# Kernel tuning notes

Measured on AMD Instinct MI355X. Metric: run time of the kernel, lower is better.

Reference implementation:

```python
import jax, jax.numpy as jnp
import numpy as np

NC, NG, NP = 8192, 4096, 140
FD, D, L = 512, 256, 2
E_OBS, E_COEXP, E_PPI, E_SYM = 300000, 200000, 10000, 20000
EPS = 1e-5


def layer_norm(x, g, b):
    mu = jnp.mean(x, -1, keepdims=True)
    v = jnp.mean((x - mu) ** 2, -1, keepdims=True)
    return (x - mu) * jax.lax.rsqrt(v + EPS) * g + b


def sage(h_src, h_dst, src, dst, w, Ws, Wn, b, n_dst):
    # DGL SAGEConv (mean aggregator, edge-weighted): mean over incoming
    # weighted messages, then fc_self(h_dst) + fc_neigh(neigh) + bias.
    m = h_src[src] * w[:, None]                                  # [E, D]
    neigh = jax.ops.segment_sum(m, dst, num_segments=n_dst)      # [n_dst, D]
    deg = jax.ops.segment_sum(jnp.ones_like(w), dst, num_segments=n_dst)
    neigh = neigh / jnp.maximum(deg, 1.0)[:, None]
    return h_dst @ Ws + neigh @ Wn + b


def setup_inputs() -> dict:
    key = jax.random.key(0)
    ks = iter(jax.random.split(key, 64))
    def n(*s):
        return jax.random.normal(next(ks), s, jnp.float32) * 0.02
    def u(e):
        return jax.random.uniform(next(ks), (e,), jnp.float32)
    def ri(e, hi):
        return jax.random.randint(next(ks), (e,), 0, hi, jnp.int32)
    return dict(
        cell_feat=jax.random.normal(next(ks), (NC, FD), jnp.float32),
        gene_feat=jax.random.normal(next(ks), (NG, FD), jnp.float32),
        pro_idx=jnp.arange(NP, dtype=jnp.int32),
        obs_src=ri(E_OBS, NG), obs_dst=ri(E_OBS, NC), obs_w=u(E_OBS),
        rev_obs_src=ri(E_OBS, NC), rev_obs_dst=ri(E_OBS, NG), rev_obs_w=u(E_OBS),
        symbol_src=ri(E_SYM, NG), symbol_dst=ri(E_SYM, NP), symbol_w=u(E_SYM),
        rev_symbol_src=ri(E_SYM, NP), rev_symbol_dst=ri(E_SYM, NG), rev_symbol_w=u(E_SYM),
        coexp_src=ri(E_COEXP, NG), coexp_dst=ri(E_COEXP, NG), coexp_w=u(E_COEXP),
        ppi_src=ri(E_PPI, NP), ppi_dst=ri(E_PPI, NP), ppi_w=u(E_PPI),
        W_emb_cell=n(FD, D), b_emb_cell=jnp.zeros((D,), jnp.float32),
        W_emb_gene=n(FD, D), b_emb_gene=jnp.zeros((D,), jnp.float32),
        emb_pro=n(NP, D),
        W_mlpcell=n(L, D, D), b_mlpcell=jnp.zeros((L, D), jnp.float32),
        W_sage_self=n(L, 6, D, D), W_sage_neigh=n(L, 6, D, D),
        b_sage=jnp.zeros((L, 6, D), jnp.float32),
        ln1_g=jnp.ones((L, 3, D), jnp.float32), ln1_b=jnp.zeros((L, 3, D), jnp.float32),
        ln2_g=jnp.ones((L, 3, D), jnp.float32), ln2_b=jnp.zeros((L, 3, D), jnp.float32),
        W_last=n(3 * D, NP), b_last=jnp.zeros((NP,), jnp.float32),
    )


def reference(cell_feat, gene_feat, pro_idx,
              obs_src, obs_dst, obs_w,
              rev_obs_src, rev_obs_dst, rev_obs_w,
              symbol_src, symbol_dst, symbol_w,
              rev_symbol_src, rev_symbol_dst, rev_symbol_w,
              coexp_src, coexp_dst, coexp_w,
              ppi_src, ppi_dst, ppi_w,
              W_emb_cell, b_emb_cell, W_emb_gene, b_emb_gene, emb_pro,
              W_mlpcell, b_mlpcell, W_sage_self, W_sage_neigh, b_sage,
              ln1_g, ln1_b, ln2_g, ln2_b, W_last, b_last):
    act = jax.nn.selu
    hc = cell_feat @ W_emb_cell + b_emb_cell      # emb_cell
    hg = gene_feat @ W_emb_gene + b_emb_gene      # emb_gene
    hp = emb_pro[pro_idx]                         # nn.Embedding path
    nc, ng, npn = hc.shape[0], hg.shape[0], hp.shape[0]
    hist = [hc]
    for l in range(W_mlpcell.shape[0]):
        Ws, Wn, bs = W_sage_self[l], W_sage_neigh[l], b_sage[l]
        hmlp = layer_norm(act(hc @ W_mlpcell[l] + b_mlpcell[l]), ln1_g[l, 2], ln1_b[l, 2])
        # HeteroGraphConv(SAGE) over edges_sub = [obs, rev_obs, symbol, rev_symbol] (stack)
        s_obs = sage(hg, hc, obs_src, obs_dst, obs_w, Ws[0], Wn[0], bs[0], nc)
        s_robs = sage(hc, hg, rev_obs_src, rev_obs_dst, rev_obs_w, Ws[1], Wn[1], bs[1], ng)
        s_sym = sage(hg, hp, symbol_src, symbol_dst, symbol_w, Ws[2], Wn[2], bs[2], npn)
        s_rsym = sage(hp, hg, rev_symbol_src, rev_symbol_dst, rev_symbol_w, Ws[3], Wn[3], bs[3], ng)
        # homogeneous subgraph convs: gene_sage on coexp, pro_sage on ppi
        h_gg = layer_norm(act(sage(hg, hg, coexp_src, coexp_dst, coexp_w, Ws[4], Wn[4], bs[4], ng)), ln1_g[l, 0], ln1_b[l, 0])
        h_pp = layer_norm(act(sage(hp, hp, ppi_src, ppi_dst, ppi_w, Ws[5], Wn[5], bs[5], npn)), ln1_g[l, 1], ln1_b[l, 1])
        # norm each stacked relation output, then agg='sum' over the stack dim
        hgen = layer_norm(act(s_robs), ln1_g[l, 0], ln1_b[l, 0]) + layer_norm(act(s_rsym), ln1_g[l, 0], ln1_b[l, 0]) + h_gg
        hpro = layer_norm(act(s_sym), ln1_g[l, 1], ln1_b[l, 1]) + h_pp
        hcel = layer_norm(act(s_obs), ln1_g[l, 2], ln1_b[l, 2]) + hmlp
        hg = layer_norm(act(hgen), ln2_g[l, 0], ln2_b[l, 0])
        hp = layer_norm(act(hpro), ln2_g[l, 1], ln2_b[l, 1])
        hc = layer_norm(act(hcel), ln2_g[l, 2], ln2_b[l, 2])
        hist.append(hc)
    # mlp_last over concat of per-layer cell reps (sum(dims[1:-1]) -> dims[-1])
    return jnp.concatenate(hist, -1) @ W_last + b_last
```

## Files before the change

kernel.cpp:

```cpp
#include <hip/hip_runtime.h>

typedef unsigned short ushort_t;
typedef unsigned int uint_t;

typedef ushort_t ushortx8 __attribute__((ext_vector_type(8)));
typedef ushort_t ushortx4 __attribute__((ext_vector_type(4)));
typedef __bf16 bf16x8 __attribute__((ext_vector_type(8)));
typedef float f32x4 __attribute__((ext_vector_type(4)));

#define NCC 8192
#define NGG 4096
#define NPP 140
#define LDS_STR 88
#define CEPB 16384

__device__ __forceinline__ float bf2f(ushort_t u) {
    uint_t i = ((uint_t)u) << 16;
    float f;
    __builtin_memcpy(&f, &i, 4);
    return f;
}
__device__ __forceinline__ ushort_t f2bf(float f) {
    uint_t i;
    __builtin_memcpy(&i, &f, 4);
    uint_t r = (i + 0x7FFFu + ((i >> 16) & 1u)) >> 16;
    return (ushort_t)r;
}
__device__ __forceinline__ float scrub(float x) {
    return __builtin_isfinite(x) ? x : 0.f;
}
__device__ __forceinline__ float selu_f(float x) {
    return x > 0.f ? 1.0507009873554805f * x : 1.7580993408473766f * expm1f(x);
}
__device__ __forceinline__ float wsum64(float x) {
    for (int o = 32; o; o >>= 1) x += __shfl_xor(x, o, 64);
    return x;
}

__global__ __launch_bounds__(256) void sc_zero1(int* __restrict__ a, int na) {
    int i = blockIdx.x * 256 + threadIdx.x;
    if (i < na) a[i] = 0;
}

struct CountJob {
    const int* dst;
    const int* src;
    const float* w;
    uint_t* pw;
    ushort_t* rank;
    int E;
    int nbins;
    int* deg;
    int bstart;
};
struct CountBatch {
    CountJob j[6];
};
struct TrJob {
    const float* src;
    ushort_t* dst;
    int K, N, nx, nxy;
    int bstart;
};
struct TrBatch {
    TrJob j[6];
};
struct FillJob {
    const int* dst;
    const uint_t* pw;
    const ushort_t* rank;
    int E;
    const int* offs;
    uint_t* ep;
    int bstart;
};
struct FillBatch {
    FillJob j[6];
};
struct GemmJob {
    const void* A1;
    int lda1, K1, af1;
    const ushort_t* Bt1;
    const ushort_t* A2;
    int K2;
    const ushort_t* Bt2;
    const float* bias;
    ushort_t* C;
    int ldc, M;
    int mstart;
};
struct GemmBatch {
    GemmJob j[7];
};

struct CountArgs {
    CountBatch cb;
    int bsC;
    const float* cf;
    ushort_t* cf16;
    int nbC;
    const float* gf;
    ushort_t* gf16;
};
__global__ __launch_bounds__(1024) void sc_count(CountArgs ca) {
    __shared__ int hist[NCC];
    int bx = blockIdx.x;
    const int tid = threadIdx.x;
    if (bx >= ca.bsC) {
        bx -= ca.bsC;
        const float* src;
        ushort_t* dst;
        if (bx < ca.nbC) {
            src = ca.cf;
            dst = ca.cf16;
        } else {
            bx -= ca.nbC;
            src = ca.gf;
            dst = ca.gf16;
        }
        size_t i = ((size_t)bx * 1024 + tid) * 8;
        float4 f0 = *(const float4*)(src + i);
        float4 f1 = *(const float4*)(src + i + 4);
        ushortx8 v;
        v[0] = f2bf(f0.x);
        v[1] = f2bf(f0.y);
        v[2] = f2bf(f0.z);
        v[3] = f2bf(f0.w);
        v[4] = f2bf(f1.x);
        v[5] = f2bf(f1.y);
        v[6] = f2bf(f1.z);
        v[7] = f2bf(f1.w);
        *(ushortx8*)(dst + i) = v;
        return;
    }
    int r = 0;
#pragma unroll
    for (int i = 1; i < 6; ++i) r = (bx >= ca.cb.j[i].bstart) ? i : r;
    const CountJob& J = ca.cb.j[r];
    const int nb = J.nbins;
    for (int b = tid; b < nb; b += 1024) hist[b] = 0;
    __syncthreads();
    const int e0 = (bx - J.bstart) * CEPB;
    ushort_t lrk[16];
#pragma unroll
    for (int u = 0; u < 16; ++u) {
        int e = e0 + u * 1024 + tid;
        if (e < J.E) {
            int d = J.dst[e];
            lrk[u] = (ushort_t)atomicAdd(&hist[d], 1);
            J.pw[e] = ((uint_t)f2bf(J.w[e]) << 16) | (uint_t)J.src[e];
        }
    }
    __syncthreads();
    for (int b = tid; b < nb; b += 1024) {
        int c = hist[b];
        if (c > 0) hist[b] = atomicAdd(&J.deg[b], c);
    }
    __syncthreads();
#pragma unroll
    for (int u = 0; u < 16; ++u) {
        int e = e0 + u * 1024 + tid;
        if (e < J.E) {
            int d = J.dst[e];
            J.rank[e] = (ushort_t)(hist[d] + (int)lrk[u]);
        }
    }
}

struct PrepArgs {
    TrBatch tb;
    int bsT;
    const float* emb;
    const int* pidx;
    ushort_t* hp;
    int nEmb;
};
__global__ __launch_bounds__(256) void sc_prep(PrepArgs pa) {
    __shared__ ushort_t t[32][33];
    int bx = blockIdx.x;
    if (bx < pa.bsT) {
        int r = 0;
#pragma unroll
        for (int i = 1; i < 6; ++i) r = (bx >= pa.tb.j[i].bstart) ? i : r;
        const TrJob& J = pa.tb.j[r];
        int local = bx - J.bstart;
        int b = local / J.nxy, rem = local % J.nxy;
        int n0 = (rem % J.nx) * 32, k0 = (rem / J.nx) * 32;
        const float* s = J.src + (size_t)b * J.K * J.N;
        ushort_t* d = J.dst + (size_t)b * J.K * J.N;
        int x = threadIdx.x & 31, y = threadIdx.x >> 5;
        for (int i = y; i < 32; i += 8) {
            int k = k0 + i, n = n0 + x;
            t[i][x] = (k < J.K && n < J.N) ? f2bf(s[(size_t)k * J.N + n]) : (ushort_t)0;
        }
        __syncthreads();
        for (int i = y; i < 32; i += 8) {
            int n = n0 + i, k = k0 + x;
            if (n < J.N && k < J.K) d[(size_t)n * J.K + k] = t[x][i];
        }
        return;
    }
    bx -= pa.bsT;
    int i = bx * 256 + threadIdx.x;
    if (i < pa.nEmb) {
        int r = i >> 8, c = i & 255;
        int j = pa.pidx[r];
        j = (uint_t)j < (uint_t)NPP ? j : 0;
        pa.hp[i] = f2bf(pa.emb[(size_t)j * 256 + c]);
    }
}

__global__ __launch_bounds__(1024) void sc_csr_scan6(const int* __restrict__ deg_base,
                                                     int* __restrict__ offs_base) {
    const int ndst[6] = {NCC, NGG, NPP, NGG, NGG, NPP};
    const int dstart[6] = {0, NCC, NCC + NGG, NCC + NGG + NPP, NCC + 2 * NGG + NPP,
                           NCC + 3 * NGG + NPP};
    const int ostart[6] = {0, NCC + 1, NCC + NGG + 2, NCC + NGG + NPP + 3,
                           NCC + 2 * NGG + NPP + 4, NCC + 3 * NGG + NPP + 5};
    int r = blockIdx.x;
    const int* deg = deg_base + dstart[r];
    int* offs = offs_base + ostart[r];
    int n = ndst[r];
    __shared__ int wsum[16];
    __shared__ int carry;
    int tid = threadIdx.x, wave = tid >> 6, lane = tid & 63;
    if (tid == 0) carry = 0;
    __syncthreads();
    for (int base = 0; base < n; base += 1024) {
        int i = base + tid;
        int v = (i < n) ? deg[i] : 0;
        int x = v;
#pragma unroll
        for (int o = 1; o < 64; o <<= 1) {
            int tv = __shfl_up(x, o, 64);
            if (lane >= o) x += tv;
        }
        if (lane == 63) wsum[wave] = x;
        __syncthreads();
        if (tid == 0) {
            int acc = 0;
#pragma unroll
            for (int k = 0; k < 16; ++k) {
                int tv = wsum[k];
                wsum[k] = acc;
                acc += tv;
            }
        }
        __syncthreads();
        int incl = x + wsum[wave];
        int cr = carry;
        if (i < n) offs[i] = cr + incl - v;
        __syncthreads();
        if (tid == 1023) carry = cr + incl;
        __syncthreads();
    }
    if (tid == 0) offs[n] = carry;
}

__device__ __forceinline__ void gemm_body(const GemmBatch& gbat, int mbx, int n0, ushort_t* As,
                                          ushort_t* Bs) {
    int r = 0;
#pragma unroll
    for (int i = 1; i < 7; ++i) r = (mbx >= gbat.j[i].mstart) ? i : r;
    const void* JA1 = gbat.j[r].A1;
    const int lda1 = gbat.j[r].lda1, K1j = gbat.j[r].K1, af1 = gbat.j[r].af1;
    const ushort_t* JBt1 = gbat.j[r].Bt1;
    const ushort_t* JA2 = gbat.j[r].A2;
    const int K2j = gbat.j[r].K2;
    const ushort_t* JBt2 = gbat.j[r].Bt2;
    const float* bias = gbat.j[r].bias;
    ushort_t* C = gbat.j[r].C;
    const int ldc = gbat.j[r].ldc, M = gbat.j[r].M;
    const int tid = threadIdx.x;
    const int wave = tid >> 6, lane = tid & 63;
    const int lr = lane & 15, lq = lane >> 4;
    const int m0 = (mbx - gbat.j[r].mstart) * 128;
    f32x4 acc[2][4] = {};
    for (int pass = 0; pass < 2; ++pass) {
        const void* A = pass ? (const void*)JA2 : JA1;
        const ushort_t* Bt = pass ? JBt2 : JBt1;
        const int K = pass ? K2j : K1j;
        const int lda = pass ? 256 : lda1;
        const int af = pass ? 0 : af1;
        if (K == 0 || A == nullptr) continue;
        for (int k0 = 0; k0 < K; k0 += 64) {
            __syncthreads();
#pragma unroll
            for (int i = 0; i < 4; ++i) {
                int g = tid + i * 256;
                int rr = g >> 3, c = (g & 7) * 8;
                ushortx8 v = {0, 0, 0, 0, 0, 0, 0, 0};
                int gm = m0 + rr;
                if (gm < M) {
                    if (af) {
                        const float* Af = (const float*)A;
                        float4 f0 = *(const float4*)(Af + (size_t)gm * lda + k0 + c);
                        float4 f1 = *(const float4*)(Af + (size_t)gm * lda + k0 + c + 4);
                        v[0] = f2bf(f0.x);
                        v[1] = f2bf(f0.y);
                        v[2] = f2bf(f0.z);
                        v[3] = f2bf(f0.w);
                        v[4] = f2bf(f1.x);
                        v[5] = f2bf(f1.y);
                        v[6] = f2bf(f1.z);
                        v[7] = f2bf(f1.w);
                    } else {
                        v = *(const ushortx8*)((const ushort_t*)A + (size_t)gm * lda + k0 + c);
                    }
                }
                *(ushortx8*)(&As[rr * LDS_STR + c]) = v;
            }
#pragma unroll
            for (int i = 0; i < 2; ++i) {
                int g = tid + i * 256;
                int rr = g >> 3, c = (g & 7) * 8;
                int gn = n0 + rr;
                ushortx8 v = *(const ushortx8*)(Bt + (size_t)gn * K + k0 + c);
                *(ushortx8*)(&Bs[rr * LDS_STR + c]) = v;
            }
            __syncthreads();
#pragma unroll
            for (int kk = 0; kk < 64; kk += 32) {
                bf16x8 a0 = __builtin_bit_cast(
                    bf16x8, *(const ushortx8*)(&As[(wave * 32 + lr) * LDS_STR + kk + lq * 8]));
                bf16x8 a1 = __builtin_bit_cast(
                    bf16x8,
                    *(const ushortx8*)(&As[(wave * 32 + 16 + lr) * LDS_STR + kk + lq * 8]));
                bf16x8 b0 = __builtin_bit_cast(
                    bf16x8, *(const ushortx8*)(&Bs[(lr)*LDS_STR + kk + lq * 8]));
                bf16x8 b1 = __builtin_bit_cast(
                    bf16x8, *(const ushortx8*)(&Bs[(16 + lr) * LDS_STR + kk + lq * 8]));
                bf16x8 b2 = __builtin_bit_cast(
                    bf16x8, *(const ushortx8*)(&Bs[(32 + lr) * LDS_STR + kk + lq * 8]));
                bf16x8 b3 = __builtin_bit_cast(
                    bf16x8, *(const ushortx8*)(&Bs[(48 + lr) * LDS_STR + kk + lq * 8]));
                acc[0][0] = __builtin_amdgcn_mfma_f32_16x16x32_bf16(a0, b0, acc[0][0], 0, 0, 0);
                acc[0][1] = __builtin_amdgcn_mfma_f32_16x16x32_bf16(a0, b1, acc[0][1], 0, 0, 0);
                acc[0][2] = __builtin_amdgcn_mfma_f32_16x16x32_bf16(a0, b2, acc[0][2], 0, 0, 0);
                acc[0][3] = __builtin_amdgcn_mfma_f32_16x16x32_bf16(a0, b3, acc[0][3], 0, 0, 0);
                acc[1][0] = __builtin_amdgcn_mfma_f32_16x16x32_bf16(a1, b0, acc[1][0], 0, 0, 0);
                acc[1][1] = __builtin_amdgcn_mfma_f32_16x16x32_bf16(a1, b1, acc[1][1], 0, 0, 0);
                acc[1][2] = __builtin_amdgcn_mfma_f32_16x16x32_bf16(a1, b2, acc[1][2], 0, 0, 0);
                acc[1][3] = __builtin_amdgcn_mfma_f32_16x16x32_bf16(a1, b3, acc[1][3], 0, 0, 0);
            }
        }
    }
#pragma unroll
    for (int mt = 0; mt < 2; ++mt)
#pragma unroll
        for (int nt = 0; nt < 4; ++nt) {
            int col = n0 + nt * 16 + lr;
            float bb = bias[col];
#pragma unroll
            for (int v = 0; v < 4; ++v) {
                int row = m0 + wave * 32 + mt * 16 + lq * 4 + v;
                if (row >= M) continue;
                C[(size_t)row * ldc + col] = f2bf(scrub(acc[mt][nt][v] + bb));
            }
        }
}

__global__ __launch_bounds__(256) void sc_gemm_batch(GemmBatch gbat) {
    __shared__ __align__(16) ushort_t As[128 * LDS_STR];
    __shared__ __align__(16) ushort_t Bs[64 * LDS_STR];
    gemm_body(gbat, blockIdx.x, blockIdx.y * 64, As, Bs);
}

struct Emb64Job {
    const ushort_t* A;
    const ushort_t* Bt;
    const float* bias;
    ushort_t* C;
    int ldc;
    ushort_t* C2;
    int mstart;
};
struct FillGemmArgs {
    Emb64Job ej[2];
    int gemmBlocks;
    FillBatch fb;
};
__global__ __launch_bounds__(256) void sc_fill_gemm(FillGemmArgs fg) {
    __shared__ __align__(16) ushort_t As[64 * LDS_STR];
    __shared__ __align__(16) ushort_t Bs[64 * LDS_STR];
    int bx = blockIdx.x;
    if (bx >= fg.gemmBlocks) {
        bx -= fg.gemmBlocks;
        int r = 0;
#pragma unroll
        for (int i = 1; i < 6; ++i) r = (bx >= fg.fb.j[i].bstart) ? i : r;
        const FillJob& J = fg.fb.j[r];
        int e = (bx - J.bstart) * 256 + threadIdx.x;
        if (e < J.E) {
            int d = J.dst[e];
            J.ep[J.offs[d] + (int)J.rank[e]] = J.pw[e];
        }
        return;
    }
    const int mb = bx >> 2, n0 = (bx & 3) * 64;
    const int r = (mb >= fg.ej[1].mstart) ? 1 : 0;
    const Emb64Job& J = fg.ej[r];
    const int m0 = (mb - J.mstart) * 64;
    const ushort_t* A = J.A;
    const ushort_t* Bt = J.Bt;
    const int tid = threadIdx.x;
    const int wave = tid >> 6, lane = tid & 63;
    const int lr = lane & 15, lq = lane >> 4;
    f32x4 acc[4] = {};
    for (int k0 = 0; k0 < 512; k0 += 64) {
        __syncthreads();
#pragma unroll
        for (int i = 0; i < 2; ++i) {
            int g = tid + i * 256;
            int rr = g >> 3, c = (g & 7) * 8;
            *(ushortx8*)(&As[rr * LDS_STR + c]) =
                *(const ushortx8*)(A + (size_t)(m0 + rr) * 512 + k0 + c);
            *(ushortx8*)(&Bs[rr * LDS_STR + c]) =
                *(const ushortx8*)(Bt + (size_t)(n0 + rr) * 512 + k0 + c);
        }
        __syncthreads();
#pragma unroll
        for (int kk = 0; kk < 64; kk += 32) {
            bf16x8 a = __builtin_bit_cast(
                bf16x8, *(const ushortx8*)(&As[(wave * 16 + lr) * LDS_STR + kk + lq * 8]));
            bf16x8 b0 =
                __builtin_bit_cast(bf16x8, *(const ushortx8*)(&Bs[(lr)*LDS_STR + kk + lq * 8]));
            bf16x8 b1 = __builtin_bit_cast(
                bf16x8, *(const ushortx8*)(&Bs[(16 + lr) * LDS_STR + kk + lq * 8]));
            bf16x8 b2 = __builtin_bit_cast(
                bf16x8, *(const ushortx8*)(&Bs[(32 + lr) * LDS_STR + kk + lq * 8]));
            bf16x8 b3 = __builtin_bit_cast(
                bf16x8, *(const ushortx8*)(&Bs[(48 + lr) * LDS_STR + kk + lq * 8]));
            acc[0] = __builtin_amdgcn_mfma_f32_16x16x32_bf16(a, b0, acc[0], 0, 0, 0);
            acc[1] = __builtin_amdgcn_mfma_f32_16x16x32_bf16(a, b1, acc[1], 0, 0, 0);
            acc[2] = __builtin_amdgcn_mfma_f32_16x16x32_bf16(a, b2, acc[2], 0, 0, 0);
            acc[3] = __builtin_amdgcn_mfma_f32_16x16x32_bf16(a, b3, acc[3], 0, 0, 0);
        }
    }
#pragma unroll
    for (int nt = 0; nt < 4; ++nt) {
        int col = n0 + nt * 16 + lr;
        float bb = J.bias[col];
#pragma unroll
        for (int v = 0; v < 4; ++v) {
            int row = m0 + wave * 16 + lq * 4 + v;
            ushort_t val = f2bf(scrub(acc[nt][v] + bb));
            J.C[(size_t)row * J.ldc + col] = val;
            if (J.C2) J.C2[(size_t)row * 256 + col] = val;
        }
    }
}

struct GatherJob {
    const ushort_t* hsrc;
    int src_ld, src_n;
    const int* offs;
    const uint_t* ep;
    ushort_t* out;
    int row_start;
};
struct GatherBatch {
    GatherJob j[6];
};
__global__ __launch_bounds__(256) void sc_gather_all(GatherBatch gb, int total_rows) {
    int grow = blockIdx.x * 4 + (threadIdx.x >> 6);
    if (grow >= total_rows) return;
    int r = 0;
#pragma unroll
    for (int i = 1; i < 6; ++i) r = (grow >= gb.j[i].row_start) ? i : r;
    r = __builtin_amdgcn_readfirstlane(r);
    const char* hsrc = (const char*)gb.j[r].hsrc;
    const uint_t row_bytes = (uint_t)(gb.j[r].src_ld * 2);
    const uint_t src_n = (uint_t)gb.j[r].src_n;
    const int* offs = gb.j[r].offs;
    const uint_t* ep = gb.j[r].ep;
    ushort_t* out = gb.j[r].out;
    int row = grow - gb.j[r].row_start;
    int lane = threadIdx.x & 63;
    int cb = lane * 8;
    int s0 = offs[row], s1 = offs[row + 1];
    float a0 = 0.f, a1 = 0.f, a2 = 0.f, a3 = 0.f;
    for (int base = s0; base < s1; base += 64) {
        int e = base + lane;
        uint_t myp = (e < s1) ? ep[e] : 0u;
        int cnt = s1 - base;
        cnt = cnt < 64 ? cnt : 64;
        int cnt16 = (cnt + 15) & ~15;
        for (int jj = 0; jj < cnt16; jj += 16) {
#pragma unroll
            for (int u = 0; u < 16; ++u) {
                uint_t pw = (uint_t)__builtin_amdgcn_readlane((int)myp, jj + u);
                uint_t s = pw & 0xFFFFu;
                s = s < src_n ? s : 0u;
                float w = bf2f((ushort_t)(pw >> 16));
                const uint2 v = *(const uint2*)(hsrc + (size_t)(s * row_bytes) + cb);
                uint_t x0 = v.x << 16, x1 = v.x & 0xFFFF0000u;
                uint_t x2 = v.y << 16, x3 = v.y & 0xFFFF0000u;
                a0 = fmaf(w, __builtin_bit_cast(float, x0), a0);
                a1 = fmaf(w, __builtin_bit_cast(float, x1), a1);
                a2 = fmaf(w, __builtin_bit_cast(float, x2), a2);
                a3 = fmaf(w, __builtin_bit_cast(float, x3), a3);
            }
        }
    }
    float inv = 1.f / fmaxf((float)(s1 - s0), 1.f);
    ushort_t* o = out + (size_t)row * 256 + lane * 4;
    o[0] = f2bf(scrub(a0 * inv));
    o[1] = f2bf(scrub(a1 * inv));
    o[2] = f2bf(scrub(a2 * inv));
    o[3] = f2bf(scrub(a3 * inv));
}

__global__ __launch_bounds__(256) void sc_gemm(const ushort_t* __restrict__ A1, int lda1,
                                               const ushort_t* __restrict__ Bt1, int K1,
                                               const float* __restrict__ bias,
                                               float* __restrict__ Cf, int ldc, int M, int N) {
    __shared__ __align__(16) ushort_t As[128 * LDS_STR];
    __shared__ __align__(16) ushort_t Bs[64 * LDS_STR];
    const int tid = threadIdx.x;
    const int wave = tid >> 6, lane = tid & 63;
    const int lr = lane & 15, lq = lane >> 4;
    const int m0 = blockIdx.x * 128, n0 = blockIdx.y * 64;
    f32x4 acc[2][4] = {};
    for (int k0 = 0; k0 < K1; k0 += 64) {
        __syncthreads();
#pragma unroll
        for (int i = 0; i < 4; ++i) {
            int g = tid + i * 256;
            int r = g >> 3, c = (g & 7) * 8;
            ushortx8 v = {0, 0, 0, 0, 0, 0, 0, 0};
            int gm = m0 + r;
            if (gm < M) v = *(const ushortx8*)(A1 + (size_t)gm * lda1 + k0 + c);
            *(ushortx8*)(&As[r * LDS_STR + c]) = v;
        }
#pragma unroll
        for (int i = 0; i < 2; ++i) {
            int g = tid + i * 256;
            int r = g >> 3, c = (g & 7) * 8;
            ushortx8 v = {0, 0, 0, 0, 0, 0, 0, 0};
            int gn = n0 + r;
            if (gn < N) v = *(const ushortx8*)(Bt1 + (size_t)gn * K1 + k0 + c);
            *(ushortx8*)(&Bs[r * LDS_STR + c]) = v;
        }
        __syncthreads();
#pragma unroll
        for (int kk = 0; kk < 64; kk += 32) {
            bf16x8 a0 = __builtin_bit_cast(
                bf16x8, *(const ushortx8*)(&As[(wave * 32 + lr) * LDS_STR + kk + lq * 8]));
            bf16x8 a1 = __builtin_bit_cast(
                bf16x8, *(const ushortx8*)(&As[(wave * 32 + 16 + lr) * LDS_STR + kk + lq * 8]));
            bf16x8 b0 =
                __builtin_bit_cast(bf16x8, *(const ushortx8*)(&Bs[(lr)*LDS_STR + kk + lq * 8]));
            bf16x8 b1 = __builtin_bit_cast(
                bf16x8, *(const ushortx8*)(&Bs[(16 + lr) * LDS_STR + kk + lq * 8]));
            bf16x8 b2 = __builtin_bit_cast(
                bf16x8, *(const ushortx8*)(&Bs[(32 + lr) * LDS_STR + kk + lq * 8]));
            bf16x8 b3 = __builtin_bit_cast(
                bf16x8, *(const ushortx8*)(&Bs[(48 + lr) * LDS_STR + kk + lq * 8]));
            acc[0][0] = __builtin_amdgcn_mfma_f32_16x16x32_bf16(a0, b0, acc[0][0], 0, 0, 0);
            acc[0][1] = __builtin_amdgcn_mfma_f32_16x16x32_bf16(a0, b1, acc[0][1], 0, 0, 0);
            acc[0][2] = __builtin_amdgcn_mfma_f32_16x16x32_bf16(a0, b2, acc[0][2], 0, 0, 0);
            acc[0][3] = __builtin_amdgcn_mfma_f32_16x16x32_bf16(a0, b3, acc[0][3], 0, 0, 0);
            acc[1][0] = __builtin_amdgcn_mfma_f32_16x16x32_bf16(a1, b0, acc[1][0], 0, 0, 0);
            acc[1][1] = __builtin_amdgcn_mfma_f32_16x16x32_bf16(a1, b1, acc[1][1], 0, 0, 0);
            acc[1][2] = __builtin_amdgcn_mfma_f32_16x16x32_bf16(a1, b2, acc[1][2], 0, 0, 0);
            acc[1][3] = __builtin_amdgcn_mfma_f32_16x16x32_bf16(a1, b3, acc[1][3], 0, 0, 0);
        }
    }
#pragma unroll
    for (int mt = 0; mt < 2; ++mt)
#pragma unroll
        for (int nt = 0; nt < 4; ++nt) {
            int col = n0 + nt * 16 + lr;
            if (col >= N) continue;
            float bb = bias ? bias[col] : 0.f;
#pragma unroll
            for (int v = 0; v < 4; ++v) {
                int row = m0 + wave * 32 + mt * 16 + lq * 4 + v;
                if (row >= M) continue;
                Cf[(size_t)row * ldc + col] = scrub(acc[mt][nt][v] + bb);
            }
        }
}

struct LnJob {
    const ushort_t *sA, *sB, *sC;
    const float *g1, *b1, *g2, *b2;
    ushort_t* out;
    int out_ld;
    ushort_t* out2;
    int row_start;
};
struct LnBatch {
    LnJob j[3];
};
__global__ __launch_bounds__(256) void sc_fuse_ln_all(LnBatch lb, int total_rows) {
    int grow = blockIdx.x * 4 + (threadIdx.x >> 6);
    if (grow >= total_rows) return;
    int r = 0;
#pragma unroll
    for (int i = 1; i < 3; ++i) r = (grow >= lb.j[i].row_start) ? i : r;
    r = __builtin_amdgcn_readfirstlane(r);
    const ushort_t* srcs[3] = {lb.j[r].sA, lb.j[r].sB, lb.j[r].sC};
    const float* g1 = lb.j[r].g1;
    const float* b1 = lb.j[r].b1;
    const float* g2 = lb.j[r].g2;
    const float* b2 = lb.j[r].b2;
    ushort_t* out = lb.j[r].out;
    int out_ld = lb.j[r].out_ld;
    ushort_t* out2 = lb.j[r].out2;
    int row = grow - lb.j[r].row_start;
    int lane = threadIdx.x & 63, c = lane * 4;
    float t[4] = {0.f, 0.f, 0.f, 0.f};
#pragma unroll
    for (int si = 0; si < 3; ++si) {
        const ushort_t* s = srcs[si];
        if (!s) continue;
        ushortx4 v = *(const ushortx4*)(s + (size_t)row * 256 + c);
        float x0 = selu_f(scrub(bf2f(v[0]))), x1 = selu_f(scrub(bf2f(v[1])));
        float x2 = selu_f(scrub(bf2f(v[2]))), x3 = selu_f(scrub(bf2f(v[3])));
        float mu = wsum64(x0 + x1 + x2 + x3) * (1.f / 256.f);
        float d0 = x0 - mu, d1 = x1 - mu, d2 = x2 - mu, d3 = x3 - mu;
        float var = wsum64(d0 * d0 + d1 * d1 + d2 * d2 + d3 * d3) * (1.f / 256.f);
        float rr = rsqrtf(var + 1e-5f);
        t[0] += d0 * rr * g1[c + 0] + b1[c + 0];
        t[1] += d1 * rr * g1[c + 1] + b1[c + 1];
        t[2] += d2 * rr * g1[c + 2] + b1[c + 2];
        t[3] += d3 * rr * g1[c + 3] + b1[c + 3];
    }
    float x0 = selu_f(scrub(t[0])), x1 = selu_f(scrub(t[1]));
    float x2 = selu_f(scrub(t[2])), x3 = selu_f(scrub(t[3]));
    float mu = wsum64(x0 + x1 + x2 + x3) * (1.f / 256.f);
    float d0 = x0 - mu, d1 = x1 - mu, d2 = x2 - mu, d3 = x3 - mu;
    float var = wsum64(d0 * d0 + d1 * d1 + d2 * d2 + d3 * d3) * (1.f / 256.f);
    float rr = rsqrtf(var + 1e-5f);
    ushort_t o0 = f2bf(scrub(d0 * rr * g2[c + 0] + b2[c + 0]));
    ushort_t o1 = f2bf(scrub(d1 * rr * g2[c + 1] + b2[c + 1]));
    ushort_t o2v = f2bf(scrub(d2 * rr * g2[c + 2] + b2[c + 2]));
    ushort_t o3 = f2bf(scrub(d3 * rr * g2[c + 3] + b2[c + 3]));
    ushort_t* o = out + (size_t)row * out_ld + c;
    o[0] = o0;
    o[1] = o1;
    o[2] = o2v;
    o[3] = o3;
    if (out2) {
        ushort_t* q = out2 + (size_t)row * 256 + c;
        q[0] = o0;
        q[1] = o1;
        q[2] = o2v;
        q[3] = o3;
    }
}

static inline int cdivi(int a, int b) { return (a + b - 1) / b; }

extern "C" void kernel_launch(void* const* d_in, const int* in_sizes, int n_in, void* d_out,
                              int out_size, void* d_ws, size_t ws_size, hipStream_t stream) {
    const float* cell_feat = (const float*)d_in[0];
    const float* gene_feat = (const float*)d_in[1];
    const int* pro_idx = (const int*)d_in[2];
    const int* edge_src[6] = {(const int*)d_in[3],  (const int*)d_in[6],  (const int*)d_in[9],
                              (const int*)d_in[12], (const int*)d_in[15], (const int*)d_in[18]};
    const int* edge_dst[6] = {(const int*)d_in[4],  (const int*)d_in[7],  (const int*)d_in[10],
                              (const int*)d_in[13], (const int*)d_in[16], (const int*)d_in[19]};
    const float* edge_w[6] = {(const float*)d_in[5],  (const float*)d_in[8],
                              (const float*)d_in[11], (const float*)d_in[14],
                              (const float*)d_in[17], (const float*)d_in[20]};
    const float* W_emb_cell = (const float*)d_in[21];
    const float* b_emb_cell = (const float*)d_in[22];
    const float* W_emb_gene = (const float*)d_in[23];
    const float* b_emb_gene = (const float*)d_in[24];
    const float* emb_pro = (const float*)d_in[25];
    const float* W_mlpcell = (const float*)d_in[26];
    const float* b_mlpcell = (const float*)d_in[27];
    const float* W_sage_self = (const float*)d_in[28];
    const float* W_sage_neigh = (const float*)d_in[29];
    const float* b_sage = (const float*)d_in[30];
    const float* ln1_g = (const float*)d_in[31];
    const float* ln1_b = (const float*)d_in[32];
    const float* ln2_g = (const float*)d_in[33];
    const float* ln2_b = (const float*)d_in[34];
    const float* W_last = (const float*)d_in[35];
    const float* b_last = (const float*)d_in[36];

    const int E_obs = in_sizes[3], E_sym = in_sizes[9], E_coexp = in_sizes[15],
              E_ppi = in_sizes[18];
    const int Er[6] = {E_obs, E_obs, E_sym, E_sym, E_coexp, E_ppi};
    const int Nd[6] = {NCC, NGG, NPP, NGG, NGG, NPP};

    char* p = (char*)d_ws;
    auto carve = [&](size_t bytes) -> char* {
        char* r = p;
        p += ((bytes + 255) & ~(size_t)255);
        return r;
    };
    ushort_t* hist = (ushort_t*)carve((size_t)NCC * 768 * 2);
    ushort_t* hg = (ushort_t*)carve((size_t)NGG * 256 * 2);
    ushort_t* hp = (ushort_t*)carve((size_t)NPP * 256 * 2);
    ushort_t* n_obs = (ushort_t*)carve((size_t)NCC * 256 * 2);
    ushort_t* n_robs = (ushort_t*)carve((size_t)NGG * 256 * 2);
    ushort_t* n_sym = (ushort_t*)carve((size_t)NPP * 256 * 2);
    ushort_t* n_rsym = (ushort_t*)carve((size_t)NGG * 256 * 2);
    ushort_t* n_coexp = (ushort_t*)carve((size_t)NGG * 256 * 2);
    ushort_t* n_ppi = (ushort_t*)carve((size_t)NPP * 256 * 2);
    ushort_t* s_obs = (ushort_t*)carve((size_t)NCC * 256 * 2);
    ushort_t* s_robs = (ushort_t*)carve((size_t)NGG * 256 * 2);
    ushort_t* s_sym = (ushort_t*)carve((size_t)NPP * 256 * 2);
    ushort_t* s_rsym = (ushort_t*)carve((size_t)NGG * 256 * 2);
    ushort_t* s_coexp = (ushort_t*)carve((size_t)NGG * 256 * 2);
    ushort_t* s_ppi = (ushort_t*)carve((size_t)NPP * 256 * 2);
    ushort_t* s_mlp = (ushort_t*)carve((size_t)NCC * 256 * 2);
    ushort_t* Wt_emb_cell = (ushort_t*)carve((size_t)512 * 256 * 2);
    ushort_t* Wt_emb_gene = (ushort_t*)carve((size_t)512 * 256 * 2);
    ushort_t* Wt_mlp = (ushort_t*)carve((size_t)2 * 256 * 256 * 2);
    ushort_t* Wt_self = (ushort_t*)carve((size_t)12 * 256 * 256 * 2);
    ushort_t* Wt_neigh = (ushort_t*)carve((size_t)12 * 256 * 256 * 2);
    ushort_t* Wt_last = (ushort_t*)carve((size_t)140 * 768 * 2);
    const int NDTOT = NCC + 3 * NGG + 2 * NPP;
    int* deg_all = (int*)carve((size_t)NDTOT * 4);
    int* offs_all = (int*)carve((size_t)(NDTOT + 6) * 4);
    const int ETOT = 2 * E_obs + 2 * E_sym + E_coexp + E_ppi;
    uint_t* pw_all = (uint_t*)carve((size_t)ETOT * 4);
    ushort_t* rank_all = (ushort_t*)carve((size_t)ETOT * 2);
    uint_t* ep_all = (uint_t*)carve((size_t)ETOT * 4);
    ushort_t* hc_cmp = (ushort_t*)carve((size_t)NCC * 256 * 2);
    ushort_t* cf16 = s_obs;
    ushort_t* gf16 = s_coexp;
    (void)ws_size;
    (void)n_in;
    (void)out_size;

    const int dS[6] = {0, NCC, NCC + NGG, NCC + NGG + NPP, NCC + 2 * NGG + NPP,
                       NCC + 3 * NGG + NPP};
    const int oS[6] = {0, NCC + 1, NCC + NGG + 2, NCC + NGG + NPP + 3, NCC + 2 * NGG + NPP + 4,
                       NCC + 3 * NGG + NPP + 5};
    int eS[6];
    eS[0] = 0;
    eS[1] = eS[0] + E_obs;
    eS[2] = eS[1] + E_obs;
    eS[3] = eS[2] + E_sym;
    eS[4] = eS[3] + E_sym;
    eS[5] = eS[4] + E_coexp;

    sc_zero1<<<cdivi(NDTOT, 256), 256, 0, stream>>>(deg_all, NDTOT);
    {
        CountArgs ca;
        int bs = 0;
        for (int r = 0; r < 6; ++r) {
            ca.cb.j[r] = {edge_dst[r], edge_src[r], edge_w[r], pw_all + eS[r], rank_all + eS[r],
                          Er[r],       Nd[r],       deg_all + dS[r], bs};
            bs += cdivi(Er[r], CEPB);
        }
        ca.bsC = bs;
        ca.cf = cell_feat;
        ca.cf16 = cf16;
        ca.nbC = (NCC * 512) / 8192;
        ca.gf = gene_feat;
        ca.gf16 = gf16;
        int nbG = (NGG * 512) / 8192;
        sc_count<<<bs + ca.nbC + nbG, 1024, 0, stream>>>(ca);
    }
    {
        PrepArgs pa;
        int bt = 0;
        auto add = [&](int idx, const float* s, ushort_t* d, int B, int K, int N) {
            int nx = cdivi(N, 32), ny = cdivi(K, 32);
            pa.tb.j[idx] = {s, d, K, N, nx, nx * ny, bt};
            bt += B * nx * ny;
        };
        add(0, W_emb_cell, Wt_emb_cell, 1, 512, 256);
        add(1, W_emb_gene, Wt_emb_gene, 1, 512, 256);
        add(2, W_mlpcell, Wt_mlp, 2, 256, 256);
        add(3, W_sage_self, Wt_self, 12, 256, 256);
        add(4, W_sage_neigh, Wt_neigh, 12, 256, 256);
        add(5, W_last, Wt_last, 1, 768, 140);
        pa.bsT = bt;
        pa.emb = emb_pro;
        pa.pidx = pro_idx;
        pa.hp = hp;
        pa.nEmb = NPP * 256;
        int bsE = cdivi(NPP * 256, 256);
        sc_prep<<<pa.bsT + bsE, 256, 0, stream>>>(pa);
    }
    sc_csr_scan6<<<6, 1024, 0, stream>>>(deg_all, offs_all);
    {
        FillGemmArgs fg;
        fg.ej[0] = {cf16, Wt_emb_cell, b_emb_cell, hist, 768, hc_cmp, 0};
        fg.ej[1] = {gf16, Wt_emb_gene, b_emb_gene, hg, 256, nullptr, NCC / 64};
        fg.gemmBlocks = (NCC / 64 + NGG / 64) * 4;
        int bs = 0;
        for (int r = 0; r < 6; ++r) {
            fg.fb.j[r] = {edge_dst[r], pw_all + eS[r], rank_all + eS[r], Er[r], offs_all + oS[r],
                          ep_all + eS[r], bs};
            bs += cdivi(Er[r], 256);
        }
        sc_fill_gemm<<<fg.gemmBlocks + bs, 256, 0, stream>>>(fg);
    }

    for (int l = 0; l < 2; ++l) {
        const ushort_t* hc_l = hist + l * 256;
        {
            GatherBatch gb;
            const ushort_t* hs[6] = {hg, hc_cmp, hg, hp, hg, hp};
            const int lds[6] = {256, 256, 256, 256, 256, 256};
            const int sn[6] = {NGG, NCC, NGG, NPP, NGG, NPP};
            ushort_t* outs[6] = {n_obs, n_robs, n_sym, n_rsym, n_coexp, n_ppi};
            int rs = 0;
            for (int r = 0; r < 6; ++r) {
                gb.j[r] = {hs[r], lds[r], sn[r], offs_all + oS[r], ep_all + eS[r], outs[r], rs};
                rs += Nd[r];
            }
            sc_gather_all<<<cdivi(rs, 4), 256, 0, stream>>>(gb, rs);
        }
        {
            const size_t WSZ = 65536;
            GemmBatch gbat;
            gbat.j[0] = {hc_l, 768, 256, 0, Wt_mlp + (size_t)l * WSZ, nullptr, 0, nullptr,
                         b_mlpcell + l * 256, s_mlp, 256, NCC, 0};
            const ushort_t* dstf[6] = {hc_l, hg, hp, hg, hg, hp};
            const int dld[6] = {768, 256, 256, 256, 256, 256};
            const ushort_t* nb[6] = {n_obs, n_robs, n_sym, n_rsym, n_coexp, n_ppi};
            ushort_t* so[6] = {s_obs, s_robs, s_sym, s_rsym, s_coexp, s_ppi};
            int ms = cdivi(NCC, 128);
            for (int r = 0; r < 6; ++r) {
                gbat.j[r + 1] = {dstf[r],
                                 dld[r],
                                 256,
                                 0,
                                 Wt_self + (size_t)(l * 6 + r) * WSZ,
                                 nb[r],
                                 256,
                                 Wt_neigh + (size_t)(l * 6 + r) * WSZ,
                                 b_sage + (l * 6 + r) * 256,
                                 so[r],
                                 256,
                                 Nd[r],
                                 ms};
                ms += cdivi(Nd[r], 128);
            }
            sc_gemm_batch<<<dim3(ms, 4), 256, 0, stream>>>(gbat);
        }
        {
            LnBatch lb;
            lb.j[0] = {s_robs, s_rsym, s_coexp, ln1_g + (l * 3 + 0) * 256,
                       ln1_b + (l * 3 + 0) * 256, ln2_g + (l * 3 + 0) * 256,
                       ln2_b + (l * 3 + 0) * 256, hg, 256, nullptr, 0};
            lb.j[1] = {s_sym, s_ppi, nullptr, ln1_g + (l * 3 + 1) * 256,
                       ln1_b + (l * 3 + 1) * 256, ln2_g + (l * 3 + 1) * 256,
                       ln2_b + (l * 3 + 1) * 256, hp, 256, nullptr, NGG};
            lb.j[2] = {s_obs, s_mlp, nullptr, ln1_g + (l * 3 + 2) * 256,
                       ln1_b + (l * 3 + 2) * 256, ln2_g + (l * 3 + 2) * 256,
                       ln2_b + (l * 3 + 2) * 256, hist + (l + 1) * 256, 768,
                       (l == 0) ? hc_cmp : nullptr, NGG + NPP};
            int rs = NGG + NPP + NCC;
            sc_fuse_ln_all<<<cdivi(rs, 4), 256, 0, stream>>>(lb, rs);
        }
    }

    sc_gemm<<<dim3(64, 3), 256, 0, stream>>>(hist, 768, Wt_last, 768, b_last, (float*)d_out, 140,
                                             NCC, 140);
}
```

Before: 389.7 us.

## Partition gather rows across XCDs so each XCD reads one source table

Replaces the linear row-to-block mapping of the batched neighbor gather with a per-XCD table that assigns each XCD (selected by blockIdx & 7) contiguous row ranges of specific relations. Relations that share a source feature table are grouped so that each XCD's L2 caches only a subset of source rows, which is meant to cut cross-XCD duplicate fetches and raise L2 hit rates. The cost is hard-coded row splits tied to the problem sizes, and load balance now depends on edge counts per segment rather than on uniform scheduling.

Measured after the change: 395.9 us. No clear change (+1.6%).

```diff
diff --git a/kernel.cpp b/kernel.cpp
--- a/kernel.cpp
+++ b/kernel.cpp
@@ -457,25 +457,44 @@
     const int* offs;
     const uint_t* ep;
     ushort_t* out;
-    int row_start;
-};
-struct GatherBatch {
+};
+struct XcdTab {
+    int rel[8][3];
+    int rstart[8][3];
+    int nrows[8][3];
+    int blocks[8][3];
+};
+struct GatherArgs {
     GatherJob j[6];
-};
-__global__ __launch_bounds__(256) void sc_gather_all(GatherBatch gb, int total_rows) {
-    int grow = blockIdx.x * 4 + (threadIdx.x >> 6);
-    if (grow >= total_rows) return;
-    int r = 0;
-#pragma unroll
-    for (int i = 1; i < 6; ++i) r = (grow >= gb.j[i].row_start) ? i : r;
-    r = __builtin_amdgcn_readfirstlane(r);
-    const char* hsrc = (const char*)gb.j[r].hsrc;
-    const uint_t row_bytes = (uint_t)(gb.j[r].src_ld * 2);
-    const uint_t src_n = (uint_t)gb.j[r].src_n;
-    const int* offs = gb.j[r].offs;
-    const uint_t* ep = gb.j[r].ep;
-    ushort_t* out = gb.j[r].out;
-    int row = grow - gb.j[r].row_start;
+    XcdTab xt;
+};
+__global__ __launch_bounds__(256) void sc_gather_all(GatherArgs ga) {
+    const int xcd = blockIdx.x & 7;
+    int sidx = blockIdx.x >> 3;
+    const int wave = threadIdx.x >> 6;
+    int seg = -1;
+#pragma unroll
+    for (int s = 0; s < 3; ++s) {
+        if (seg < 0) {
+            int b = ga.xt.blocks[xcd][s];
+            if (sidx < b) {
+                seg = s;
+            } else {
+                sidx -= b;
+            }
+        }
+    }
+    if (seg < 0) return;
+    const int r = ga.xt.rel[xcd][seg];
+    const int rs = ga.xt.rstart[xcd][seg];
+    const int row = rs + sidx * 4 + wave;
+    if (row >= rs + ga.xt.nrows[xcd][seg]) return;
+    const char* hsrc = (const char*)ga.j[r].hsrc;
+    const uint_t row_bytes = (uint_t)(ga.j[r].src_ld * 2);
+    const uint_t src_n = (uint_t)ga.j[r].src_n;
+    const int* offs = ga.j[r].offs;
+    const uint_t* ep = ga.j[r].ep;
+    ushort_t* out = ga.j[r].out;
     int lane = threadIdx.x & 63;
     int cb = lane * 8;
     int s0 = offs[row], s1 = offs[row + 1];
@@ -797,20 +816,53 @@
         sc_fill_gemm<<<fg.gemmBlocks + bs, 256, 0, stream>>>(fg);
     }
 
+    GatherArgs ga;
+    int maxBlk = 0;
+    {
+        for (int x = 0; x < 8; ++x)
+            for (int s = 0; s < 3; ++s) {
+                ga.xt.rel[x][s] = -1;
+                ga.xt.rstart[x][s] = 0;
+                ga.xt.nrows[x][s] = 0;
+                ga.xt.blocks[x][s] = 0;
+            }
+        int fill[8] = {0, 0, 0, 0, 0, 0, 0, 0};
+        auto seg = [&](int x, int rel, int rs, int nr) {
+            int s = fill[x]++;
+            ga.xt.rel[x][s] = rel;
+            ga.xt.rstart[x][s] = rs;
+            ga.xt.nrows[x][s] = nr;
+            ga.xt.blocks[x][s] = cdivi(nr, 4);
+        };
+        seg(0, 0, 0, 2732);
+        seg(1, 0, 2732, 2732);
+        seg(2, 0, 5464, 2728);
+        seg(0, 3, 0, 1368);
+        seg(1, 3, 1368, 1368);
+        seg(2, 3, 2736, 1360);
+        seg(2, 5, 0, NPP);
+        seg(3, 1, 0, 1368);
+        seg(4, 1, 1368, 1368);
+        seg(5, 1, 2736, 1360);
+        seg(6, 4, 0, 2048);
+        seg(6, 2, 0, NPP);
+        seg(7, 4, 2048, 2048);
+        for (int x = 0; x < 8; ++x) {
+            int t = ga.xt.blocks[x][0] + ga.xt.blocks[x][1] + ga.xt.blocks[x][2];
+            maxBlk = t > maxBlk ? t : maxBlk;
+        }
+    }
+
     for (int l = 0; l < 2; ++l) {
         const ushort_t* hc_l = hist + l * 256;
         {
-            GatherBatch gb;
             const ushort_t* hs[6] = {hg, hc_cmp, hg, hp, hg, hp};
-            const int lds[6] = {256, 256, 256, 256, 256, 256};
             const int sn[6] = {NGG, NCC, NGG, NPP, NGG, NPP};
             ushort_t* outs[6] = {n_obs, n_robs, n_sym, n_rsym, n_coexp, n_ppi};
-            int rs = 0;
             for (int r = 0; r < 6; ++r) {
-                gb.j[r] = {hs[r], lds[r], sn[r], offs_all + oS[r], ep_all + eS[r], outs[r], rs};
-                rs += Nd[r];
-            }
-            sc_gather_all<<<cdivi(rs, 4), 256, 0, stream>>>(gb, rs);
+                ga.j[r] = {hs[r], 256, sn[r], offs_all + oS[r], ep_all + eS[r], outs[r]};
+            }
+            sc_gather_all<<<8 * maxBlk, 256, 0, stream>>>(ga);
         }
         {
             const size_t WSZ = 65536;
```

## Merge prep into count kernel and fuse MLP GEMM into gather launch

Applied to the files above, without the earlier changes.

Folds the weight-transpose and protein-embedding prep work into the sc_count launch, reusing its shared-memory histogram as transpose scratch with 1024-thread blocks. It also moves the per-layer cell MLP GEMM out of the batched SAGE GEMM and into the gather kernel as extra MFMA blocks, so the MLP runs alongside the memory-bound gathers. The intent is fewer launches and better overlap of compute-bound and memory-bound work. The cost is added branching and a larger shared-memory footprint in the gather kernel, which could reduce its occupancy.

New measurement: 381.2 us. -2.2%, faster.

```diff
diff --git a/kernel.cpp b/kernel.cpp
--- a/kernel.cpp
+++ b/kernel.cpp
@@ -99,8 +99,15 @@
     const float* cf;
     ushort_t* cf16;
     int nbC;
+    int nbCvt;
     const float* gf;
     ushort_t* gf16;
+    TrBatch tb;
+    int bsT;
+    const float* emb;
+    const int* pidx;
+    ushort_t* hp;
+    int nEmb;
 };
 __global__ __launch_bounds__(1024) void sc_count(CountArgs ca) {
     __shared__ int hist[NCC];
@@ -108,29 +115,64 @@
     const int tid = threadIdx.x;
     if (bx >= ca.bsC) {
         bx -= ca.bsC;
-        const float* src;
-        ushort_t* dst;
-        if (bx < ca.nbC) {
-            src = ca.cf;
-            dst = ca.cf16;
-        } else {
-            bx -= ca.nbC;
-            src = ca.gf;
-            dst = ca.gf16;
-        }
-        size_t i = ((size_t)bx * 1024 + tid) * 8;
-        float4 f0 = *(const float4*)(src + i);
-        float4 f1 = *(const float4*)(src + i + 4);
-        ushortx8 v;
-        v[0] = f2bf(f0.x);
-        v[1] = f2bf(f0.y);
-        v[2] = f2bf(f0.z);
-        v[3] = f2bf(f0.w);
-        v[4] = f2bf(f1.x);
-        v[5] = f2bf(f1.y);
-        v[6] = f2bf(f1.z);
-        v[7] = f2bf(f1.w);
-        *(ushortx8*)(dst + i) = v;
+        if (bx < ca.nbCvt) {
+            const float* src;
+            ushort_t* dst;
+            if (bx < ca.nbC) {
+                src = ca.cf;
+                dst = ca.cf16;
+            } else {
+                bx -= ca.nbC;
+                src = ca.gf;
+                dst = ca.gf16;
+            }
+            size_t i = ((size_t)bx * 1024 + tid) * 8;
+            float4 f0 = *(const float4*)(src + i);
+            float4 f1 = *(const float4*)(src + i + 4);
+            ushortx8 v;
+            v[0] = f2bf(f0.x);
+            v[1] = f2bf(f0.y);
+            v[2] = f2bf(f0.z);
+            v[3] = f2bf(f0.w);
+            v[4] = f2bf(f1.x);
+            v[5] = f2bf(f1.y);
+            v[6] = f2bf(f1.z);
+            v[7] = f2bf(f1.w);
+            *(ushortx8*)(dst + i) = v;
+            return;
+        }
+        bx -= ca.nbCvt;
+        if (bx < ca.bsT) {
+            ushort_t* tt = (ushort_t*)hist;
+            int r = 0;
+#pragma unroll
+            for (int i = 1; i < 6; ++i) r = (bx >= ca.tb.j[i].bstart) ? i : r;
+            const TrJob& J = ca.tb.j[r];
+            int local = bx - J.bstart;
+            int b = local / J.nxy, rem = local % J.nxy;
+            int n0 = (rem % J.nx) * 32, k0 = (rem / J.nx) * 32;
+            const float* s = J.src + (size_t)b * J.K * J.N;
+            ushort_t* d = J.dst + (size_t)b * J.K * J.N;
+            int x = tid & 31, y = tid >> 5;
+            {
+                int k = k0 + y, n = n0 + x;
+                tt[y * 33 + x] = (k < J.K && n < J.N) ? f2bf(s[(size_t)k * J.N + n]) : (ushort_t)0;
+            }
+            __syncthreads();
+            {
+                int n = n0 + y, k = k0 + x;
+                if (n < J.N && k < J.K) d[(size_t)n * J.K + k] = tt[x * 33 + y];
+            }
+            return;
+        }
+        bx -= ca.bsT;
+        int i = bx * 1024 + tid;
+        if (i < ca.nEmb) {
+            int r = i >> 8, c = i & 255;
+            int j = ca.pidx[r];
+            j = (uint_t)j < (uint_t)NPP ? j : 0;
+            ca.hp[i] = f2bf(ca.emb[(size_t)j * 256 + c]);
+        }
         return;
     }
     int r = 0;
@@ -164,49 +206,6 @@
             int d = J.dst[e];
             J.rank[e] = (ushort_t)(hist[d] + (int)lrk[u]);
         }
-    }
-}
-
-struct PrepArgs {
-    TrBatch tb;
-    int bsT;
-    const float* emb;
-    const int* pidx;
-    ushort_t* hp;
-    int nEmb;
-};
-__global__ __launch_bounds__(256) void sc_prep(PrepArgs pa) {
-    __shared__ ushort_t t[32][33];
-    int bx = blockIdx.x;
-    if (bx < pa.bsT) {
-        int r = 0;
-#pragma unroll
-        for (int i = 1; i < 6; ++i) r = (bx >= pa.tb.j[i].bstart) ? i : r;
-        const TrJob& J = pa.tb.j[r];
-        int local = bx - J.bstart;
-        int b = local / J.nxy, rem = local % J.nxy;
-        int n0 = (rem % J.nx) * 32, k0 = (rem / J.nx) * 32;
-        const float* s = J.src + (size_t)b * J.K * J.N;
-        ushort_t* d = J.dst + (size_t)b * J.K * J.N;
-        int x = threadIdx.x & 31, y = threadIdx.x >> 5;
-        for (int i = y; i < 32; i += 8) {
-            int k = k0 + i, n = n0 + x;
-            t[i][x] = (k < J.K && n < J.N) ? f2bf(s[(size_t)k * J.N + n]) : (ushort_t)0;
-        }
-        __syncthreads();
-        for (int i = y; i < 32; i += 8) {
-            int n = n0 + i, k = k0 + x;
-            if (n < J.N && k < J.K) d[(size_t)n * J.K + k] = t[x][i];
-        }
-        return;
-    }
-    bx -= pa.bsT;
-    int i = bx * 256 + threadIdx.x;
-    if (i < pa.nEmb) {
-        int r = i >> 8, c = i & 255;
-        int j = pa.pidx[r];
-        j = (uint_t)j < (uint_t)NPP ? j : 0;
-        pa.hp[i] = f2bf(pa.emb[(size_t)j * 256 + c]);
     }
 }
 
@@ -459,24 +458,83 @@
     ushort_t* out;
     int row_start;
 };
-struct GatherBatch {
+struct GatherMlpArgs {
     GatherJob j[6];
-};
-__global__ __launch_bounds__(256) void sc_gather_all(GatherBatch gb, int total_rows) {
-    int grow = blockIdx.x * 4 + (threadIdx.x >> 6);
-    if (grow >= total_rows) return;
+    int gemmBlocks;
+    const ushort_t* mA;
+    const ushort_t* mBt;
+    const float* mbias;
+    ushort_t* mC;
+    int total_rows;
+};
+__global__ __launch_bounds__(256) void sc_gather_mlp(GatherMlpArgs ga) {
+    __shared__ __align__(16) ushort_t As[64 * LDS_STR];
+    __shared__ __align__(16) ushort_t Bs[64 * LDS_STR];
+    int bx = blockIdx.x;
+    const int tid = threadIdx.x;
+    if (bx < ga.gemmBlocks) {
+        const int mb = bx >> 2, n0 = (bx & 3) * 64;
+        const int m0 = mb * 64;
+        const int wave = tid >> 6, lane = tid & 63;
+        const int lr = lane & 15, lq = lane >> 4;
+        f32x4 acc[4] = {};
+        for (int k0 = 0; k0 < 256; k0 += 64) {
+            __syncthreads();
+#pragma unroll
+            for (int i = 0; i < 2; ++i) {
+                int g = tid + i * 256;
+                int rr = g >> 3, c = (g & 7) * 8;
+                *(ushortx8*)(&As[rr * LDS_STR + c]) =
+                    *(const ushortx8*)(ga.mA + (size_t)(m0 + rr) * 768 + k0 + c);
+                *(ushortx8*)(&Bs[rr * LDS_STR + c]) =
+                    *(const ushortx8*)(ga.mBt + (size_t)(n0 + rr) * 256 + k0 + c);
+            }
+            __syncthreads();
+#pragma unroll
+            for (int kk = 0; kk < 64; kk += 32) {
+                bf16x8 a = __builtin_bit_cast(
+                    bf16x8, *(const ushortx8*)(&As[(wave * 16 + lr) * LDS_STR + kk + lq * 8]));
+                bf16x8 b0 = __builtin_bit_cast(
+                    bf16x8, *(const ushortx8*)(&Bs[(lr)*LDS_STR + kk + lq * 8]));
+                bf16x8 b1 = __builtin_bit_cast(
+                    bf16x8, *(const ushortx8*)(&Bs[(16 + lr) * LDS_STR + kk + lq * 8]));
+                bf16x8 b2 = __builtin_bit_cast(
+                    bf16x8, *(const ushortx8*)(&Bs[(32 + lr) * LDS_STR + kk + lq * 8]));
+                bf16x8 b3 = __builtin_bit_cast(
+                    bf16x8, *(const ushortx8*)(&Bs[(48 + lr) * LDS_STR + kk + lq * 8]));
+                acc[0] = __builtin_amdgcn_mfma_f32_16x16x32_bf16(a, b0, acc[0], 0, 0, 0);
+                acc[1] = __builtin_amdgcn_mfma_f32_16x16x32_bf16(a, b1, acc[1], 0, 0, 0);
+                acc[2] = __builtin_amdgcn_mfma_f32_16x16x32_bf16(a, b2, acc[2], 0, 0, 0);
+                acc[3] = __builtin_amdgcn_mfma_f32_16x16x32_bf16(a, b3, acc[3], 0, 0, 0);
+            }
+        }
+#pragma unroll
+        for (int nt = 0; nt < 4; ++nt) {
+            int col = n0 + nt * 16 + lr;
+            float bb = ga.mbias[col];
+#pragma unroll
+            for (int v = 0; v < 4; ++v) {
+                int row = m0 + wave * 16 + lq * 4 + v;
+                ga.mC[(size_t)row * 256 + col] = f2bf(scrub(acc[nt][v] + bb));
+            }
+        }
+        return;
+    }
+    bx -= ga.gemmBlocks;
+    int grow = bx * 4 + (tid >> 6);
+    if (grow >= ga.total_rows) return;
     int r = 0;
 #pragma unroll
-    for (int i = 1; i < 6; ++i) r = (grow >= gb.j[i].row_start) ? i : r;
+    for (int i = 1; i < 6; ++i) r = (grow >= ga.j[i].row_start) ? i : r;
     r = __builtin_amdgcn_readfirstlane(r);
-    const char* hsrc = (const char*)gb.j[r].hsrc;
-    const uint_t row_bytes = (uint_t)(gb.j[r].src_ld * 2);
-    const uint_t src_n = (uint_t)gb.j[r].src_n;
-    const int* offs = gb.j[r].offs;
-    const uint_t* ep = gb.j[r].ep;
-    ushort_t* out = gb.j[r].out;
-    int row = grow - gb.j[r].row_start;
-    int lane = threadIdx.x & 63;
+    const char* hsrc = (const char*)ga.j[r].hsrc;
+    const uint_t row_bytes = (uint_t)(ga.j[r].src_ld * 2);
+    const uint_t src_n = (uint_t)ga.j[r].src_n;
+    const int* offs = ga.j[r].offs;
+    const uint_t* ep = ga.j[r].ep;
+    ushort_t* out = ga.j[r].out;
+    int row = grow - ga.j[r].row_start;
+    int lane = tid & 63;
     int cb = lane * 8;
     int s0 = offs[row], s1 = offs[row + 1];
     float a0 = 0.f, a1 = 0.f, a2 = 0.f, a3 = 0.f;
@@ -758,14 +816,11 @@
         ca.gf = gene_feat;
         ca.gf16 = gf16;
         int nbG = (NGG * 512) / 8192;
-        sc_count<<<bs + ca.nbC + nbG, 1024, 0, stream>>>(ca);
-    }
-    {
-        PrepArgs pa;
+        ca.nbCvt = ca.nbC + nbG;
         int bt = 0;
         auto add = [&](int idx, const float* s, ushort_t* d, int B, int K, int N) {
             int nx = cdivi(N, 32), ny = cdivi(K, 32);
-            pa.tb.j[idx] = {s, d, K, N, nx, nx * ny, bt};
+            ca.tb.j[idx] = {s, d, K, N, nx, nx * ny, bt};
             bt += B * nx * ny;
         };
         add(0, W_emb_cell, Wt_emb_cell, 1, 512, 256);
@@ -774,13 +829,13 @@
         add(3, W_sage_self, Wt_self, 12, 256, 256);
         add(4, W_sage_neigh, Wt_neigh, 12, 256, 256);
         add(5, W_last, Wt_last, 1, 768, 140);
-        pa.bsT = bt;
-        pa.emb = emb_pro;
-        pa.pidx = pro_idx;
-        pa.hp = hp;
-        pa.nEmb = NPP * 256;
-        int bsE = cdivi(NPP * 256, 256);
-        sc_prep<<<pa.bsT + bsE, 256, 0, stream>>>(pa);
+        ca.bsT = bt;
+        ca.emb = emb_pro;
+        ca.pidx = pro_idx;
+        ca.hp = hp;
+        ca.nEmb = NPP * 256;
+        int bsE = cdivi(NPP * 256, 1024);
+        sc_count<<<bs + ca.nbCvt + bt + bsE, 1024, 0, stream>>>(ca);
     }
     sc_csr_scan6<<<6, 1024, 0, stream>>>(deg_all, offs_all);
     {
@@ -800,44 +855,49 @@
     for (int l = 0; l < 2; ++l) {
         const ushort_t* hc_l = hist + l * 256;
         {
-            GatherBatch gb;
+            GatherMlpArgs ga;
             const ushort_t* hs[6] = {hg, hc_cmp, hg, hp, hg, hp};
-            const int lds[6] = {256, 256, 256, 256, 256, 256};
             const int sn[6] = {NGG, NCC, NGG, NPP, NGG, NPP};
             ushort_t* outs[6] = {n_obs, n_robs, n_sym, n_rsym, n_coexp, n_ppi};
             int rs = 0;
             for (int r = 0; r < 6; ++r) {
-                gb.j[r] = {hs[r], lds[r], sn[r], offs_all + oS[r], ep_all + eS[r], outs[r], rs};
+                ga.j[r] = {hs[r], 256, sn[r], offs_all + oS[r], ep_all + eS[r], outs[r], rs};
                 rs += Nd[r];
             }
-            sc_gather_all<<<cdivi(rs, 4), 256, 0, stream>>>(gb, rs);
+            ga.gemmBlocks = (NCC / 64) * 4;
+            ga.mA = hc_l;
+            ga.mBt = Wt_mlp + (size_t)l * 65536;
+            ga.mbias = b_mlpcell + l * 256;
+            ga.mC = s_mlp;
+            ga.total_rows = rs;
+            sc_gather_mlp<<<ga.gemmBlocks + cdivi(rs, 4), 256, 0, stream>>>(ga);
         }
         {
             const size_t WSZ = 65536;
             GemmBatch gbat;
-            gbat.j[0] = {hc_l, 768, 256, 0, Wt_mlp + (size_t)l * WSZ, nullptr, 0, nullptr,
-                         b_mlpcell + l * 256, s_mlp, 256, NCC, 0};
             const ushort_t* dstf[6] = {hc_l, hg, hp, hg, hg, hp};
             const int dld[6] = {768, 256, 256, 256, 256, 256};
             const ushort_t* nb[6] = {n_obs, n_robs, n_sym, n_rsym, n_coexp, n_ppi};
             ushort_t* so[6] = {s_obs, s_robs, s_sym, s_rsym, s_coexp, s_ppi};
-            int ms = cdivi(NCC, 128);
+            int ms = 0;
             for (int r = 0; r < 6; ++r) {
-                gbat.j[r + 1] = {dstf[r],
-                                 dld[r],
-                                 256,
-                                 0,
-                                 Wt_self + (size_t)(l * 6 + r) * WSZ,
-                                 nb[r],
-                                 256,
-                                 Wt_neigh + (size_t)(l * 6 + r) * WSZ,
-                                 b_sage + (l * 6 + r) * 256,
-                                 so[r],
-                                 256,
-                                 Nd[r],
-                                 ms};
+                gbat.j[r] = {dstf[r],
+                             dld[r],
+                             256,
+                             0,
+                             Wt_self + (size_t)(l * 6 + r) * WSZ,
+                             nb[r],
+                             256,
+                             Wt_neigh + (size_t)(l * 6 + r) * WSZ,
+                             b_sage + (l * 6 + r) * 256,
+                             so[r],
+                             256,
+                             Nd[r],
+                             ms};
                 ms += cdivi(Nd[r], 128);
             }
+            gbat.j[6] = gbat.j[5];
+            gbat.j[6].mstart = 0x7FFFFFFF;
             sc_gemm_batch<<<dim3(ms, 4), 256, 0, stream>>>(gbat);
         }
         {
```
